# Kernel tuning notes

Measured on AMD Instinct MI355X. Metric: run time of the kernel, lower is better.

## Reference

```python
import jax, jax.numpy as jnp
import numpy as np

N, E, D, L, B = 50000, 800000, 128, 3, 256
BN_EPS = 1e-5


def _bn(h, g, b):
    # BatchNorm1d training-mode math over the node axis (biased variance)
    mu = jnp.mean(h, axis=0)
    var = jnp.mean(jnp.square(h - mu), axis=0)
    return (h - mu) * jax.lax.rsqrt(var + BN_EPS) * g + b


def setup_inputs() -> dict:
    key = jax.random.key(0)
    ks = jax.random.split(key, 6)
    scale = 1.0 / np.sqrt(D).astype(np.float32)
    return {
        "x": jax.random.normal(ks[0], (N, D), dtype=jnp.float32),
        "edge_index": jax.random.randint(ks[1], (2, E), 0, N, dtype=jnp.int32),
        "batch": jnp.sort(jax.random.randint(ks[2], (N,), 0, B, dtype=jnp.int32)),
        "W1": jax.random.normal(ks[3], (L, D, D), dtype=jnp.float32) * scale,
        "b1": jnp.zeros((L, D), jnp.float32),
        "g1": jnp.ones((L, D), jnp.float32),
        "be1": jnp.zeros((L, D), jnp.float32),
        "W2": jax.random.normal(ks[4], (L, D, D), dtype=jnp.float32) * scale,
        "b2": jnp.zeros((L, D), jnp.float32),
        "g2": jnp.ones((L, D), jnp.float32),
        "be2": jnp.zeros((L, D), jnp.float32),
    }


def reference(x, edge_index, batch, W1, b1, g1, be1, W2, b2, g2, be2):
    src, dst = edge_index[0], edge_index[1]
    h = x
    for i in range(L):
        # GINConv (eps=0): h' = nn((1+eps)*h + sum_{j in N(i)} h_j)
        agg = jax.ops.segment_sum(h[src], dst, num_segments=N)  # [N, D]
        h = h + agg
        # nn_layer: Linear -> BN -> ReLU -> Linear
        h = jax.nn.relu(_bn(h @ W1[i] + b1[i], g1[i], be1[i])) @ W2[i] + b2[i]
        # outer BatchNorm + ReLU (dropout is identity in eval)
        h = jax.nn.relu(_bn(h, g2[i], be2[i]))
    # global_add_pool over graphs
    return jax.ops.segment_sum(h, batch, num_segments=B)  # [B, D]
```

## Files before the change

kernel.cpp:

```cpp
#include <hip/hip_runtime.h>

constexpr int kN = 50000;
constexpr int kE = 800000;
constexpr int kD = 128;
constexpr int kB = 256;
constexpr int kL = 3;
constexpr float kEps = 1e-5f;

constexpr int kShift = 7;
constexpr int kNBuk = (kN + 127) >> 7;
constexpr int kEPB = 8192;
constexpr int kNBinBlk = (kE + kEPB - 1) / kEPB;

constexpr int kPxc = kN * kD / 8;
constexpr int kPbnd = kPxc + kN + 1;
constexpr int kPw1 = kPbnd + kL * kD * kD;
constexpr int kPw2 = kPw1 + kL * kD * kD;
constexpr int kPrepThreadBlks = (kPw2 + 255) / 256;

typedef __attribute__((ext_vector_type(8))) short short8;
typedef __attribute__((ext_vector_type(4))) float f32x4;

__device__ __forceinline__ float4 bnrelu4(float4 v, float4 sc, float4 sh) {
  float4 r;
  r.x = fmaxf(fmaf(v.x, sc.x, sh.x), 0.f);
  r.y = fmaxf(fmaf(v.y, sc.y, sh.y), 0.f);
  r.z = fmaxf(fmaf(v.z, sc.z, sh.z), 0.f);
  r.w = fmaxf(fmaf(v.w, sc.w, sh.w), 0.f);
  return r;
}

__device__ __forceinline__ void acc4(float4& a, const float4& v) {
  a.x += v.x; a.y += v.y; a.z += v.z; a.w += v.w;
}
__device__ __forceinline__ void accsq4(float4& a, const float4& v) {
  a.x = fmaf(v.x, v.x, a.x); a.y = fmaf(v.y, v.y, a.y);
  a.z = fmaf(v.z, v.z, a.z); a.w = fmaf(v.w, v.w, a.w);
}

__device__ __forceinline__ unsigned int f2bf(float x) {
  unsigned int u = __float_as_uint(x);
  u = u + 0x7FFFu + ((u >> 16) & 1u);
  return u >> 16;
}
__device__ __forceinline__ float bf2f(unsigned int lo16) {
  return __uint_as_float(lo16 << 16);
}

__device__ __forceinline__ void bnmake(float su, float sq, float ga, float be,
                                       float& sc, float& sh) {
  float mu = su * (1.f / kN);
  float var = fmaf(-mu, mu, sq * (1.f / kN));
  float s = ga * rsqrtf(var + kEps);
  sc = s;
  sh = fmaf(-mu, s, be);
}

__global__ __launch_bounds__(256) void k_prep(
    const float* __restrict__ x, const int* __restrict__ ei,
    const int* __restrict__ bat, const float* __restrict__ W1,
    const float* __restrict__ W2, unsigned short* __restrict__ x16,
    int* __restrict__ bhist, int* __restrict__ gstart,
    unsigned short* __restrict__ Wf1, unsigned short* __restrict__ Wf2) {
  __shared__ int cnt[kNBuk];
  if (blockIdx.x < (unsigned)kNBinBlk) {
    const int tid = threadIdx.x;
    const int e0 = blockIdx.x * kEPB;
    for (int t = tid; t < kNBuk; t += 256) cnt[t] = 0;
    __syncthreads();
#pragma unroll
    for (int i = 0; i < 32; ++i) {
      int e = e0 + i * 256 + tid;
      if (e < kE) atomicAdd(&cnt[ei[kE + e] >> kShift], 1);
    }
    __syncthreads();
    for (int t = tid; t < kNBuk; t += 256) {
      int c = cnt[t];
      if (c) atomicAdd(&bhist[t], c);
    }
    return;
  }
  int idx = (blockIdx.x - kNBinBlk) * 256 + threadIdx.x;
  if (idx < kPxc) {
    const float* ap = x + (size_t)idx * 8;
    float4 v0 = *reinterpret_cast<const float4*>(ap);
    float4 v1 = *reinterpret_cast<const float4*>(ap + 4);
    short8 u;
    u[0] = (short)f2bf(v0.x); u[1] = (short)f2bf(v0.y);
    u[2] = (short)f2bf(v0.z); u[3] = (short)f2bf(v0.w);
    u[4] = (short)f2bf(v1.x); u[5] = (short)f2bf(v1.y);
    u[6] = (short)f2bf(v1.z); u[7] = (short)f2bf(v1.w);
    *reinterpret_cast<short8*>(x16 + (size_t)idx * 8) = u;
  } else if (idx < kPbnd) {
    int n = idx - kPxc;
    int b = (n < kN) ? bat[n] : kB;
    int bp = (n > 0) ? bat[n - 1] : -1;
    for (int g = bp + 1; g <= b; ++g) gstart[g] = n;
  } else if (idx < kPw2) {
    const float* W = (idx < kPw1) ? W1 : W2;
    unsigned short* Wf = (idx < kPw1) ? Wf1 : Wf2;
    int id2 = idx - ((idx < kPw1) ? kPbnd : kPw1);
    int m = id2 & (kD * kD - 1);
    int w = id2 >> 14;
    int k = m >> 7, col = m & 127;
    int kb = k >> 5, cb = col >> 4;
    int lane = (col & 15) + 16 * ((k & 31) >> 3);
    int j = k & 7;
    Wf[(size_t)w * kD * kD + ((size_t)(kb * 8 + cb) * 64 + lane) * 8 + j] =
        (unsigned short)f2bf(W[id2]);
  }
}

__global__ __launch_bounds__(512) void k_scanB(const int* __restrict__ bhist,
                                               int* __restrict__ bstart,
                                               int* __restrict__ bcur) {
  __shared__ int wsum[8];
  const int tid = threadIdx.x;
  const int lane = tid & 63, wid = tid >> 6;
  int v = (tid < kNBuk) ? bhist[tid] : 0;
  int inc = v;
#pragma unroll
  for (int off = 1; off < 64; off <<= 1) {
    int t = __shfl_up(inc, off);
    if (lane >= off) inc += t;
  }
  if (lane == 63) wsum[wid] = inc;
  __syncthreads();
  int wpre = 0;
#pragma unroll
  for (int k = 0; k < 8; ++k) {
    int t = wsum[k];
    if (k < wid) wpre += t;
  }
  int excl = wpre + inc - v;
  if (tid <= kNBuk) {
    bstart[tid] = excl;
    if (tid < kNBuk) bcur[tid] = excl;
  }
}

__global__ __launch_bounds__(256) void k_binpairs(
    const int* __restrict__ ei, int* __restrict__ bcur,
    unsigned int* __restrict__ pairs) {
  __shared__ int cnt[kNBuk];
  __shared__ int base[kNBuk];
  const int tid = threadIdx.x;
  const int e0 = blockIdx.x * kEPB;
  for (int t = tid; t < kNBuk; t += 256) cnt[t] = 0;
  __syncthreads();
  unsigned int dr[32];
#pragma unroll
  for (int i = 0; i < 32; ++i) {
    int e = e0 + i * 256 + tid;
    unsigned int v = 0xFFFFFFFFu;
    if (e < kE) {
      int d = ei[kE + e];
      int r = atomicAdd(&cnt[d >> kShift], 1);
      v = ((unsigned int)d << 16) | (unsigned int)r;
    }
    dr[i] = v;
  }
  __syncthreads();
  for (int t = tid; t < kNBuk; t += 256) {
    int c = cnt[t];
    base[t] = (c > 0) ? atomicAdd(&bcur[t], c) : 0;
  }
  __syncthreads();
#pragma unroll
  for (int i = 0; i < 32; ++i) {
    unsigned int v = dr[i];
    if (v == 0xFFFFFFFFu) continue;
    int e = e0 + i * 256 + tid;
    unsigned int s = (unsigned int)ei[e];
    int b = (int)(v >> 16) >> kShift;
    int pos = base[b] + (int)(v & 0xFFFFu);
    pairs[pos] = (v & 0xFFFF0000u) | s;
  }
}

__global__ __launch_bounds__(256) void k_csrfill(
    const unsigned int* __restrict__ pairs, const int* __restrict__ bstart,
    int* __restrict__ rowptr, int* __restrict__ srcs) {
  __shared__ int cnt[128];
  __shared__ int cur[128];
  __shared__ int w0tot;
  const int b = blockIdx.x;
  const int tid = threadIdx.x;
  const int n0 = b << kShift;
  const int pb = bstart[b];
  const int pe = bstart[b + 1];
  if (tid < 128) cnt[tid] = 0;
  __syncthreads();
  for (int p = pb + tid; p < pe; p += 256)
    atomicAdd(&cnt[(int)(pairs[p] >> 16) - n0], 1);
  __syncthreads();
  int v = 0, inc = 0;
  if (tid < 128) {
    v = cnt[tid];
    inc = v;
#pragma unroll
    for (int off = 1; off < 64; off <<= 1) {
      int t = __shfl_up(inc, off);
      if ((tid & 63) >= off) inc += t;
    }
    if (tid == 63) w0tot = inc;
  }
  __syncthreads();
  if (tid < 128) {
    int excl = inc - v + ((tid >= 64) ? w0tot : 0);
    int n = n0 + tid;
    if (n <= kN) rowptr[n] = pb + excl;
    cur[tid] = pb + excl;
  }
  __syncthreads();
  for (int p = pb + tid; p < pe; p += 256) {
    unsigned int u = pairs[p];
    int local = (int)(u >> 16) - n0;
    int pos = atomicAdd(&cur[local], 1);
    srcs[pos] = (int)(u & 0xFFFFu);
  }
}

template <bool BN>
__global__ __launch_bounds__(256) void k_gather(
    const unsigned int* __restrict__ h16, const int* __restrict__ rowptr,
    const int* __restrict__ srcs, const float* __restrict__ stats,
    const float* __restrict__ gam, const float* __restrict__ bet,
    unsigned int* __restrict__ agg16) {
  const int node = blockIdx.x * 4 + (threadIdx.x >> 6);
  const int lane = threadIdx.x & 63;
  float scx, scy, shx, shy;
  if (BN) {
    int c = lane * 2;
    bnmake(stats[c], stats[kD + c], gam[c], bet[c], scx, shx);
    bnmake(stats[c + 1], stats[kD + c + 1], gam[c + 1], bet[c + 1], scy, shy);
  }
  unsigned int u = h16[(size_t)node * 64 + lane];
  float ax = bf2f(u & 0xFFFFu), ay = __uint_as_float(u & 0xFFFF0000u);
  if (BN) {
    ax = fmaxf(fmaf(ax, scx, shx), 0.f);
    ay = fmaxf(fmaf(ay, scy, shy), 0.f);
  }
  const int beg = __builtin_amdgcn_readfirstlane(rowptr[node]);
  const int end = __builtin_amdgcn_readfirstlane(rowptr[node + 1]);
  int j = beg;
  for (; j + 4 <= end; j += 4) {
    int s0 = srcs[j + 0];
    int s1 = srcs[j + 1];
    int s2 = srcs[j + 2];
    int s3 = srcs[j + 3];
    unsigned int v0 = h16[(size_t)s0 * 64 + lane];
    unsigned int v1 = h16[(size_t)s1 * 64 + lane];
    unsigned int v2 = h16[(size_t)s2 * 64 + lane];
    unsigned int v3 = h16[(size_t)s3 * 64 + lane];
    float x0 = bf2f(v0 & 0xFFFFu), y0 = __uint_as_float(v0 & 0xFFFF0000u);
    float x1 = bf2f(v1 & 0xFFFFu), y1 = __uint_as_float(v1 & 0xFFFF0000u);
    float x2 = bf2f(v2 & 0xFFFFu), y2 = __uint_as_float(v2 & 0xFFFF0000u);
    float x3 = bf2f(v3 & 0xFFFFu), y3 = __uint_as_float(v3 & 0xFFFF0000u);
    if (BN) {
      x0 = fmaxf(fmaf(x0, scx, shx), 0.f); y0 = fmaxf(fmaf(y0, scy, shy), 0.f);
      x1 = fmaxf(fmaf(x1, scx, shx), 0.f); y1 = fmaxf(fmaf(y1, scy, shy), 0.f);
      x2 = fmaxf(fmaf(x2, scx, shx), 0.f); y2 = fmaxf(fmaf(y2, scy, shy), 0.f);
      x3 = fmaxf(fmaf(x3, scx, shx), 0.f); y3 = fmaxf(fmaf(y3, scy, shy), 0.f);
    }
    ax += (x0 + x1) + (x2 + x3);
    ay += (y0 + y1) + (y2 + y3);
  }
  for (; j < end; ++j) {
    int s = srcs[j];
    unsigned int v = h16[(size_t)s * 64 + lane];
    float vx = bf2f(v & 0xFFFFu), vy = __uint_as_float(v & 0xFFFF0000u);
    if (BN) {
      vx = fmaxf(fmaf(vx, scx, shx), 0.f);
      vy = fmaxf(fmaf(vy, scy, shy), 0.f);
    }
    ax += vx;
    ay += vy;
  }
  agg16[(size_t)node * 64 + lane] = f2bf(ax) | (f2bf(ay) << 16);
}

__global__ __launch_bounds__(256) void k_gemm(
    const unsigned short* __restrict__ A16, const unsigned short* __restrict__ Wf,
    const float* __restrict__ bias, const float* __restrict__ statsA,
    const float* __restrict__ gamA, const float* __restrict__ betA,
    unsigned short* __restrict__ Y16,
    float* __restrict__ s_sum, float* __restrict__ s_ss) {
  union SMem {
    unsigned short af[32 * 64 * 8];
    float epi[64 * 132];
  };
  __shared__ SMem sm;

  const int tid = threadIdx.x;
  const int w = tid >> 6;
  const int lane = tid & 63;
  const int row0 = blockIdx.x * 128;

  short8 bfr[4][2];
#pragma unroll
  for (int kb = 0; kb < 4; ++kb)
#pragma unroll
    for (int c = 0; c < 2; ++c)
      bfr[kb][c] = *reinterpret_cast<const short8*>(
          Wf + ((size_t)(kb * 8 + (2 * w + c)) * 64 + lane) * 8);

  {
    const int rlow = tid >> 4;
    const int k0 = (tid & 15) * 8;
    const int kb = k0 >> 5;
    const int lif = rlow + 16 * ((k0 & 31) >> 3);
    float4 sc0, sc1, sh0, sh1;
    if (statsA != nullptr) {
      float4 su0 = *reinterpret_cast<const float4*>(statsA + k0);
      float4 su1 = *reinterpret_cast<const float4*>(statsA + k0 + 4);
      float4 sq0 = *reinterpret_cast<const float4*>(statsA + kD + k0);
      float4 sq1 = *reinterpret_cast<const float4*>(statsA + kD + k0 + 4);
      float4 ga0 = *reinterpret_cast<const float4*>(gamA + k0);
      float4 ga1 = *reinterpret_cast<const float4*>(gamA + k0 + 4);
      float4 be0 = *reinterpret_cast<const float4*>(betA + k0);
      float4 be1 = *reinterpret_cast<const float4*>(betA + k0 + 4);
      bnmake(su0.x, sq0.x, ga0.x, be0.x, sc0.x, sh0.x);
      bnmake(su0.y, sq0.y, ga0.y, be0.y, sc0.y, sh0.y);
      bnmake(su0.z, sq0.z, ga0.z, be0.z, sc0.z, sh0.z);
      bnmake(su0.w, sq0.w, ga0.w, be0.w, sc0.w, sh0.w);
      bnmake(su1.x, sq1.x, ga1.x, be1.x, sc1.x, sh1.x);
      bnmake(su1.y, sq1.y, ga1.y, be1.y, sc1.y, sh1.y);
      bnmake(su1.z, sq1.z, ga1.z, be1.z, sc1.z, sh1.z);
      bnmake(su1.w, sq1.w, ga1.w, be1.w, sc1.w, sh1.w);
    }
#pragma unroll
    for (int i = 0; i < 8; ++i) {
      int grow = row0 + rlow + 16 * i;
      short8 u = (short8)0;
      if (grow < kN) {
        u = *reinterpret_cast<const short8*>(A16 + (size_t)grow * kD + k0);
        if (statsA != nullptr) {
          float4 v0, v1;
          v0.x = bf2f((unsigned short)u[0]); v0.y = bf2f((unsigned short)u[1]);
          v0.z = bf2f((unsigned short)u[2]); v0.w = bf2f((unsigned short)u[3]);
          v1.x = bf2f((unsigned short)u[4]); v1.y = bf2f((unsigned short)u[5]);
          v1.z = bf2f((unsigned short)u[6]); v1.w = bf2f((unsigned short)u[7]);
          v0 = bnrelu4(v0, sc0, sh0);
          v1 = bnrelu4(v1, sc1, sh1);
          u[0] = (short)f2bf(v0.x); u[1] = (short)f2bf(v0.y);
          u[2] = (short)f2bf(v0.z); u[3] = (short)f2bf(v0.w);
          u[4] = (short)f2bf(v1.x); u[5] = (short)f2bf(v1.y);
          u[6] = (short)f2bf(v1.z); u[7] = (short)f2bf(v1.w);
        }
      }
      int frag = i * 4 + kb;
      *reinterpret_cast<short8*>(&sm.af[((size_t)frag * 64 + lif) * 8]) = u;
    }
  }
  __syncthreads();

  f32x4 acc[8][2];
#pragma unroll
  for (int rb = 0; rb < 8; ++rb) {
    acc[rb][0] = (f32x4){0.f, 0.f, 0.f, 0.f};
    acc[rb][1] = (f32x4){0.f, 0.f, 0.f, 0.f};
  }
#pragma unroll
  for (int kb = 0; kb < 4; ++kb) {
    short8 afr[8];
#pragma unroll
    for (int rb = 0; rb < 8; ++rb)
      afr[rb] = *reinterpret_cast<const short8*>(
          &sm.af[((size_t)(rb * 4 + kb) * 64 + lane) * 8]);
#pragma unroll
    for (int rb = 0; rb < 8; ++rb) {
      acc[rb][0] = __builtin_amdgcn_mfma_f32_16x16x32_bf16(afr[rb], bfr[kb][0],
                                                           acc[rb][0], 0, 0, 0);
      acc[rb][1] = __builtin_amdgcn_mfma_f32_16x16x32_bf16(afr[rb], bfr[kb][1],
                                                           acc[rb][1], 0, 0, 0);
    }
  }

  const int col4 = tid & 31;
  const int rowg = tid >> 5;
  float4 b4 = reinterpret_cast<const float4*>(bias)[col4];
  float4 ss = make_float4(0.f, 0.f, 0.f, 0.f);
  float4 qq = make_float4(0.f, 0.f, 0.f, 0.f);

#pragma unroll
  for (int p = 0; p < 2; ++p) {
    __syncthreads();
#pragma unroll
    for (int rb4 = 0; rb4 < 4; ++rb4) {
      int rb = p * 4 + rb4;
#pragma unroll
      for (int c = 0; c < 2; ++c) {
#pragma unroll
        for (int j = 0; j < 4; ++j) {
          sm.epi[(size_t)(rb4 * 16 + (lane >> 4) * 4 + j) * 132 +
                 w * 32 + c * 16 + (lane & 15)] = acc[rb][c][j];
        }
      }
    }
    __syncthreads();
#pragma unroll
    for (int i = 0; i < 8; ++i) {
      int lrow = rowg * 8 + i;
      int grow = row0 + p * 64 + lrow;
      float4 v = *reinterpret_cast<float4*>(&sm.epi[(size_t)lrow * 132 + col4 * 4]);
      acc4(v, b4);
      if (grow < kN) {
        uint2 pk;
        pk.x = f2bf(v.x) | (f2bf(v.y) << 16);
        pk.y = f2bf(v.z) | (f2bf(v.w) << 16);
        *reinterpret_cast<uint2*>(Y16 + (size_t)grow * kD + col4 * 4) = pk;
        acc4(ss, v);
        accsq4(qq, v);
      }
    }
  }

  __syncthreads();
  *reinterpret_cast<float4*>(&sm.epi[(size_t)rowg * 128 + col4 * 4]) = ss;
  *reinterpret_cast<float4*>(&sm.epi[1024 + (size_t)rowg * 128 + col4 * 4]) = qq;
  __syncthreads();
  if (tid < kD) {
    float s = 0.f;
#pragma unroll
    for (int j = 0; j < 8; ++j) s += sm.epi[j * 128 + tid];
    atomicAdd(&s_sum[tid], s);
  } else {
    int c = tid - kD;
    float s = 0.f;
#pragma unroll
    for (int j = 0; j < 8; ++j) s += sm.epi[1024 + j * 128 + c];
    atomicAdd(&s_ss[c], s);
  }
}

__global__ __launch_bounds__(256) void k_pool(
    const unsigned short* __restrict__ h16, const int* __restrict__ gstart,
    const float* __restrict__ stats, const float* __restrict__ gam,
    const float* __restrict__ bet, float* __restrict__ out) {
  const int g = blockIdx.x;
  const int q = threadIdx.x & 31;
  const int r = threadIdx.x >> 5;
  const int s = gstart[g], e = gstart[g + 1];
  float4 sc, sh;
  {
    int c = q * 4;
    bnmake(stats[c + 0], stats[kD + c + 0], gam[c + 0], bet[c + 0], sc.x, sh.x);
    bnmake(stats[c + 1], stats[kD + c + 1], gam[c + 1], bet[c + 1], sc.y, sh.y);
    bnmake(stats[c + 2], stats[kD + c + 2], gam[c + 2], bet[c + 2], sc.z, sh.z);
    bnmake(stats[c + 3], stats[kD + c + 3], gam[c + 3], bet[c + 3], sc.w, sh.w);
  }
  float4 acc = make_float4(0.f, 0.f, 0.f, 0.f);
  for (int n = s + r; n < e; n += 8) {
    uint2 u = *reinterpret_cast<const uint2*>(h16 + (size_t)n * kD + q * 4);
    float4 v;
    v.x = bf2f(u.x & 0xFFFFu);
    v.y = __uint_as_float(u.x & 0xFFFF0000u);
    v.z = bf2f(u.y & 0xFFFFu);
    v.w = __uint_as_float(u.y & 0xFFFF0000u);
    acc4(acc, bnrelu4(v, sc, sh));
  }
  __shared__ float4 red[8][32];
  red[r][q] = acc;
  __syncthreads();
  if (r == 0) {
    float4 t = acc;
#pragma unroll
    for (int j = 1; j < 8; ++j) acc4(t, red[j][q]);
    reinterpret_cast<float4*>(out)[(size_t)g * 32 + q] = t;
  }
}

extern "C" void kernel_launch(void* const* d_in, const int* in_sizes, int n_in,
                              void* d_out, int out_size, void* d_ws, size_t ws_size,
                              hipStream_t stream) {
  const float* x   = (const float*)d_in[0];
  const int*   ei  = (const int*)d_in[1];
  const int*   bat = (const int*)d_in[2];
  const float* W1  = (const float*)d_in[3];
  const float* b1  = (const float*)d_in[4];
  const float* g1  = (const float*)d_in[5];
  const float* be1 = (const float*)d_in[6];
  const float* W2  = (const float*)d_in[7];
  const float* b2  = (const float*)d_in[8];
  const float* g2  = (const float*)d_in[9];
  const float* be2 = (const float*)d_in[10];
  float* out = (float*)d_out;

  char* p = (char*)d_ws;
  float* wsf = (float*)p;                       p += 16384;
  unsigned short* x16 = (unsigned short*)p;     p += (size_t)kN * kD * 2;
  unsigned short* bufA = (unsigned short*)p;    p += (size_t)kN * kD * 2;
  unsigned short* bufB = (unsigned short*)p;    p += (size_t)kN * kD * 2;
  unsigned short* Wf1 = (unsigned short*)p;     p += (size_t)kL * kD * kD * 2;
  unsigned short* Wf2 = (unsigned short*)p;     p += (size_t)kL * kD * kD * 2;
  int* rowptr = (int*)p;                        p += (kN + 2) * 4;
  int* bhist = (int*)p;                         p += (kNBuk + 1) * 4;
  int* bstart = (int*)p;                        p += (kNBuk + 1) * 4;
  int* bcur = (int*)p;                          p += (kNBuk + 1) * 4;
  int* gstart = (int*)p;                        p += (kB + 2) * 4;
  unsigned int* pairs = (unsigned int*)p;       p += (size_t)kE * 4;
  int* srcs = (int*)p;                          p += (size_t)kE * 4;

  (void)hipMemsetAsync(wsf, 0, 6 * 512 * sizeof(float), stream);
  (void)hipMemsetAsync(bhist, 0, kNBuk * sizeof(int), stream);

  k_prep<<<kNBinBlk + kPrepThreadBlks, 256, 0, stream>>>(x, ei, bat, W1, W2, x16,
                                                         bhist, gstart, Wf1, Wf2);
  k_scanB<<<1, 512, 0, stream>>>(bhist, bstart, bcur);
  k_binpairs<<<kNBinBlk, 256, 0, stream>>>(ei, bcur, pairs);
  k_csrfill<<<kNBuk, 256, 0, stream>>>(pairs, bstart, rowptr, srcs);

  const unsigned short* curH = x16;
  const float* curStats = nullptr;
  const float* curGam = nullptr;
  const float* curBet = nullptr;
  const int ngemm = (kN + 127) / 128;

  unsigned short* aggBuf = bufA;
  unsigned short* yBuf = bufB;

  for (int l = 0; l < kL; ++l) {
    if (curStats == nullptr)
      k_gather<false><<<kN / 4, 256, 0, stream>>>(
          (const unsigned int*)curH, rowptr, srcs, nullptr, nullptr, nullptr,
          (unsigned int*)aggBuf);
    else
      k_gather<true><<<kN / 4, 256, 0, stream>>>(
          (const unsigned int*)curH, rowptr, srcs, curStats, curGam, curBet,
          (unsigned int*)aggBuf);

    float* st1 = wsf + (size_t)(l * 2 + 0) * 512;
    k_gemm<<<ngemm, 256, 0, stream>>>(aggBuf, Wf1 + (size_t)l * kD * kD,
                                      b1 + l * kD, nullptr, nullptr, nullptr,
                                      yBuf, st1, st1 + kD);

    float* st2 = wsf + (size_t)(l * 2 + 1) * 512;
    k_gemm<<<ngemm, 256, 0, stream>>>(yBuf, Wf2 + (size_t)l * kD * kD,
                                      b2 + l * kD, st1, g1 + l * kD, be1 + l * kD,
                                      aggBuf, st2, st2 + kD);

    curH = aggBuf;
    curStats = st2;
    curGam = g2 + l * kD;
    curBet = be2 + l * kD;
    unsigned short* tmp = aggBuf;
    aggBuf = yBuf;
    yBuf = tmp;
  }

  k_pool<<<kB, 256, 0, stream>>>(curH, gstart, curStats, curGam, curBet, out);
}
```

Measured before the change: 293.6 us.

## Fuse neighbor gather into first GEMM and drop memsets and global histogram atomics

The separate gather kernel is replaced by k_gemmg, which aggregates each node's neighbors straight into LDS as bf16 MFMA A-fragments and then runs the first linear layer. This removes one kernel launch per layer and the round trip of the aggregated tensor through global memory. The edge-bucket histogram now writes per-block counts that the scan kernel sums, replacing global atomics, and the stats buffer is zeroed inside k_prep instead of by two memset calls. The gather now uses 16 lanes per row with uint4 loads, so memory-level parallelism changes and the MFMA stage waits on irregular gather latency within each block.

```diff
diff --git a/kernel.cpp b/kernel.cpp
--- a/kernel.cpp
+++ b/kernel.cpp
@@ -16,7 +16,8 @@
 constexpr int kPbnd = kPxc + kN + 1;
 constexpr int kPw1 = kPbnd + kL * kD * kD;
 constexpr int kPw2 = kPw1 + kL * kD * kD;
-constexpr int kPrepThreadBlks = (kPw2 + 255) / 256;
+constexpr int kPzero = kPw2 + 768;
+constexpr int kPrepThreadBlks = (kPzero + 255) / 256;
 
 typedef __attribute__((ext_vector_type(8))) short short8;
 typedef __attribute__((ext_vector_type(4))) float f32x4;
@@ -46,6 +47,9 @@
 __device__ __forceinline__ float bf2f(unsigned int lo16) {
   return __uint_as_float(lo16 << 16);
 }
+__device__ __forceinline__ float bfhi(unsigned int u) {
+  return __uint_as_float(u & 0xFFFF0000u);
+}
 
 __device__ __forceinline__ void bnmake(float su, float sq, float ga, float be,
                                        float& sc, float& sh) {
@@ -56,12 +60,34 @@
   sh = fmaf(-mu, s, be);
 }
 
+template <bool BN>
+__device__ __forceinline__ void rowadd(float* a, uint4 v, const float* sc,
+                                       const float* sh) {
+  float t0 = bf2f(v.x & 0xFFFFu), t1 = bfhi(v.x);
+  float t2 = bf2f(v.y & 0xFFFFu), t3 = bfhi(v.y);
+  float t4 = bf2f(v.z & 0xFFFFu), t5 = bfhi(v.z);
+  float t6 = bf2f(v.w & 0xFFFFu), t7 = bfhi(v.w);
+  if (BN) {
+    t0 = fmaxf(fmaf(t0, sc[0], sh[0]), 0.f);
+    t1 = fmaxf(fmaf(t1, sc[1], sh[1]), 0.f);
+    t2 = fmaxf(fmaf(t2, sc[2], sh[2]), 0.f);
+    t3 = fmaxf(fmaf(t3, sc[3], sh[3]), 0.f);
+    t4 = fmaxf(fmaf(t4, sc[4], sh[4]), 0.f);
+    t5 = fmaxf(fmaf(t5, sc[5], sh[5]), 0.f);
+    t6 = fmaxf(fmaf(t6, sc[6], sh[6]), 0.f);
+    t7 = fmaxf(fmaf(t7, sc[7], sh[7]), 0.f);
+  }
+  a[0] += t0; a[1] += t1; a[2] += t2; a[3] += t3;
+  a[4] += t4; a[5] += t5; a[6] += t6; a[7] += t7;
+}
+
 __global__ __launch_bounds__(256) void k_prep(
     const float* __restrict__ x, const int* __restrict__ ei,
     const int* __restrict__ bat, const float* __restrict__ W1,
     const float* __restrict__ W2, unsigned short* __restrict__ x16,
-    int* __restrict__ bhist, int* __restrict__ gstart,
-    unsigned short* __restrict__ Wf1, unsigned short* __restrict__ Wf2) {
+    int* __restrict__ bcnt, int* __restrict__ gstart,
+    unsigned short* __restrict__ Wf1, unsigned short* __restrict__ Wf2,
+    float* __restrict__ wsf) {
   __shared__ int cnt[kNBuk];
   if (blockIdx.x < (unsigned)kNBinBlk) {
     const int tid = threadIdx.x;
@@ -74,10 +100,8 @@
       if (e < kE) atomicAdd(&cnt[ei[kE + e] >> kShift], 1);
     }
     __syncthreads();
-    for (int t = tid; t < kNBuk; t += 256) {
-      int c = cnt[t];
-      if (c) atomicAdd(&bhist[t], c);
-    }
+    for (int t = tid; t < kNBuk; t += 256)
+      bcnt[blockIdx.x * kNBuk + t] = cnt[t];
     return;
   }
   int idx = (blockIdx.x - kNBinBlk) * 256 + threadIdx.x;
@@ -108,16 +132,22 @@
     int j = k & 7;
     Wf[(size_t)w * kD * kD + ((size_t)(kb * 8 + cb) * 64 + lane) * 8 + j] =
         (unsigned short)f2bf(W[id2]);
-  }
-}
-
-__global__ __launch_bounds__(512) void k_scanB(const int* __restrict__ bhist,
+  } else if (idx < kPzero) {
+    int z = idx - kPw2;
+    reinterpret_cast<float4*>(wsf)[z] = make_float4(0.f, 0.f, 0.f, 0.f);
+  }
+}
+
+__global__ __launch_bounds__(512) void k_scanB(const int* __restrict__ bcnt,
                                                int* __restrict__ bstart,
                                                int* __restrict__ bcur) {
   __shared__ int wsum[8];
   const int tid = threadIdx.x;
   const int lane = tid & 63, wid = tid >> 6;
-  int v = (tid < kNBuk) ? bhist[tid] : 0;
+  int v = 0;
+  if (tid < kNBuk) {
+    for (int blk = 0; blk < kNBinBlk; ++blk) v += bcnt[blk * kNBuk + tid];
+  }
   int inc = v;
 #pragma unroll
   for (int off = 1; off < 64; off <<= 1) {
@@ -222,62 +252,154 @@
 }
 
 template <bool BN>
-__global__ __launch_bounds__(256) void k_gather(
+__global__ __launch_bounds__(256) void k_gemmg(
     const unsigned int* __restrict__ h16, const int* __restrict__ rowptr,
-    const int* __restrict__ srcs, const float* __restrict__ stats,
+    const int* __restrict__ srcs, const unsigned short* __restrict__ Wf,
+    const float* __restrict__ bias, const float* __restrict__ stats,
     const float* __restrict__ gam, const float* __restrict__ bet,
-    unsigned int* __restrict__ agg16) {
-  const int node = blockIdx.x * 4 + (threadIdx.x >> 6);
-  const int lane = threadIdx.x & 63;
-  float scx, scy, shx, shy;
+    unsigned short* __restrict__ Y16,
+    float* __restrict__ s_sum, float* __restrict__ s_ss) {
+  union SMem {
+    unsigned short af[32 * 64 * 8];
+    float epi[64 * 132];
+  };
+  __shared__ SMem sm;
+
+  const int tid = threadIdx.x;
+  const int w = tid >> 6;
+  const int lane = tid & 63;
+  const int row0 = blockIdx.x * 128;
+
+  const int rlow = tid >> 4;
+  const int c4 = tid & 15;
+  const int kb = c4 >> 2;
+  const int lif = rlow + 16 * (c4 & 3);
+
+  float sc[8], sh[8];
   if (BN) {
-    int c = lane * 2;
-    bnmake(stats[c], stats[kD + c], gam[c], bet[c], scx, shx);
-    bnmake(stats[c + 1], stats[kD + c + 1], gam[c + 1], bet[c + 1], scy, shy);
-  }
-  unsigned int u = h16[(size_t)node * 64 + lane];
-  float ax = bf2f(u & 0xFFFFu), ay = __uint_as_float(u & 0xFFFF0000u);
-  if (BN) {
-    ax = fmaxf(fmaf(ax, scx, shx), 0.f);
-    ay = fmaxf(fmaf(ay, scy, shy), 0.f);
-  }
-  const int beg = __builtin_amdgcn_readfirstlane(rowptr[node]);
-  const int end = __builtin_amdgcn_readfirstlane(rowptr[node + 1]);
-  int j = beg;
-  for (; j + 4 <= end; j += 4) {
-    int s0 = srcs[j + 0];
-    int s1 = srcs[j + 1];
-    int s2 = srcs[j + 2];
-    int s3 = srcs[j + 3];
-    unsigned int v0 = h16[(size_t)s0 * 64 + lane];
-    unsigned int v1 = h16[(size_t)s1 * 64 + lane];
-    unsigned int v2 = h16[(size_t)s2 * 64 + lane];
-    unsigned int v3 = h16[(size_t)s3 * 64 + lane];
-    float x0 = bf2f(v0 & 0xFFFFu), y0 = __uint_as_float(v0 & 0xFFFF0000u);
-    float x1 = bf2f(v1 & 0xFFFFu), y1 = __uint_as_float(v1 & 0xFFFF0000u);
-    float x2 = bf2f(v2 & 0xFFFFu), y2 = __uint_as_float(v2 & 0xFFFF0000u);
-    float x3 = bf2f(v3 & 0xFFFFu), y3 = __uint_as_float(v3 & 0xFFFF0000u);
-    if (BN) {
-      x0 = fmaxf(fmaf(x0, scx, shx), 0.f); y0 = fmaxf(fmaf(y0, scy, shy), 0.f);
-      x1 = fmaxf(fmaf(x1, scx, shx), 0.f); y1 = fmaxf(fmaf(y1, scy, shy), 0.f);
-      x2 = fmaxf(fmaf(x2, scx, shx), 0.f); y2 = fmaxf(fmaf(y2, scy, shy), 0.f);
-      x3 = fmaxf(fmaf(x3, scx, shx), 0.f); y3 = fmaxf(fmaf(y3, scy, shy), 0.f);
-    }
-    ax += (x0 + x1) + (x2 + x3);
-    ay += (y0 + y1) + (y2 + y3);
-  }
-  for (; j < end; ++j) {
-    int s = srcs[j];
-    unsigned int v = h16[(size_t)s * 64 + lane];
-    float vx = bf2f(v & 0xFFFFu), vy = __uint_as_float(v & 0xFFFF0000u);
-    if (BN) {
-      vx = fmaxf(fmaf(vx, scx, shx), 0.f);
-      vy = fmaxf(fmaf(vy, scy, shy), 0.f);
-    }
-    ax += vx;
-    ay += vy;
-  }
-  agg16[(size_t)node * 64 + lane] = f2bf(ax) | (f2bf(ay) << 16);
+    int k0 = c4 * 8;
+#pragma unroll
+    for (int q = 0; q < 8; ++q)
+      bnmake(stats[k0 + q], stats[kD + k0 + q], gam[k0 + q], bet[k0 + q],
+             sc[q], sh[q]);
+  }
+
+#pragma unroll
+  for (int i = 0; i < 8; ++i) {
+    int row = row0 + rlow + 16 * i;
+    float a[8] = {0.f, 0.f, 0.f, 0.f, 0.f, 0.f, 0.f, 0.f};
+    if (row < kN) {
+      uint4 vs = *reinterpret_cast<const uint4*>(h16 + (size_t)row * 64 + c4 * 4);
+      rowadd<BN>(a, vs, sc, sh);
+      int beg = rowptr[row];
+      int end = rowptr[row + 1];
+      int j = beg;
+      for (; j + 2 <= end; j += 2) {
+        int s0 = srcs[j];
+        int s1 = srcs[j + 1];
+        uint4 v0 = *reinterpret_cast<const uint4*>(h16 + (size_t)s0 * 64 + c4 * 4);
+        uint4 v1 = *reinterpret_cast<const uint4*>(h16 + (size_t)s1 * 64 + c4 * 4);
+        rowadd<BN>(a, v0, sc, sh);
+        rowadd<BN>(a, v1, sc, sh);
+      }
+      if (j < end) {
+        int s0 = srcs[j];
+        uint4 v0 = *reinterpret_cast<const uint4*>(h16 + (size_t)s0 * 64 + c4 * 4);
+        rowadd<BN>(a, v0, sc, sh);
+      }
+    }
+    short8 u;
+#pragma unroll
+    for (int q = 0; q < 8; ++q) u[q] = (short)f2bf(a[q]);
+    *reinterpret_cast<short8*>(&sm.af[((size_t)(i * 4 + kb) * 64 + lif) * 8]) = u;
+  }
+
+  short8 bfr[4][2];
+#pragma unroll
+  for (int kk = 0; kk < 4; ++kk)
+#pragma unroll
+    for (int c = 0; c < 2; ++c)
+      bfr[kk][c] = *reinterpret_cast<const short8*>(
+          Wf + ((size_t)(kk * 8 + (2 * w + c)) * 64 + lane) * 8);
+  __syncthreads();
+
+  f32x4 acc[8][2];
+#pragma unroll
+  for (int rb = 0; rb < 8; ++rb) {
+    acc[rb][0] = (f32x4){0.f, 0.f, 0.f, 0.f};
+    acc[rb][1] = (f32x4){0.f, 0.f, 0.f, 0.f};
+  }
+#pragma unroll
+  for (int kk = 0; kk < 4; ++kk) {
+    short8 afr[8];
+#pragma unroll
+    for (int rb = 0; rb < 8; ++rb)
+      afr[rb] = *reinterpret_cast<const short8*>(
+          &sm.af[((size_t)(rb * 4 + kk) * 64 + lane) * 8]);
+#pragma unroll
+    for (int rb = 0; rb < 8; ++rb) {
+      acc[rb][0] = __builtin_amdgcn_mfma_f32_16x16x32_bf16(afr[rb], bfr[kk][0],
+                                                           acc[rb][0], 0, 0, 0);
+      acc[rb][1] = __builtin_amdgcn_mfma_f32_16x16x32_bf16(afr[rb], bfr[kk][1],
+                                                           acc[rb][1], 0, 0, 0);
+    }
+  }
+
+  const int col4 = tid & 31;
+  const int rowg = tid >> 5;
+  float4 b4 = reinterpret_cast<const float4*>(bias)[col4];
+  float4 ss = make_float4(0.f, 0.f, 0.f, 0.f);
+  float4 qq = make_float4(0.f, 0.f, 0.f, 0.f);
+
+#pragma unroll
+  for (int p = 0; p < 2; ++p) {
+    __syncthreads();
+#pragma unroll
+    for (int rb4 = 0; rb4 < 4; ++rb4) {
+      int rb = p * 4 + rb4;
+#pragma unroll
+      for (int c = 0; c < 2; ++c) {
+#pragma unroll
+        for (int j = 0; j < 4; ++j) {
+          sm.epi[(size_t)(rb4 * 16 + (lane >> 4) * 4 + j) * 132 +
+                 w * 32 + c * 16 + (lane & 15)] = acc[rb][c][j];
+        }
+      }
+    }
+    __syncthreads();
+#pragma unroll
+    for (int i = 0; i < 8; ++i) {
+      int lrow = rowg * 8 + i;
+      int grow = row0 + p * 64 + lrow;
+      float4 v = *reinterpret_cast<float4*>(&sm.epi[(size_t)lrow * 132 + col4 * 4]);
+      acc4(v, b4);
+      if (grow < kN) {
+        uint2 pk;
+        pk.x = f2bf(v.x) | (f2bf(v.y) << 16);
+        pk.y = f2bf(v.z) | (f2bf(v.w) << 16);
+        *reinterpret_cast<uint2*>(Y16 + (size_t)grow * kD + col4 * 4) = pk;
+        acc4(ss, v);
+        accsq4(qq, v);
+      }
+    }
+  }
+
+  __syncthreads();
+  *reinterpret_cast<float4*>(&sm.epi[(size_t)rowg * 128 + col4 * 4]) = ss;
+  *reinterpret_cast<float4*>(&sm.epi[1024 + (size_t)rowg * 128 + col4 * 4]) = qq;
+  __syncthreads();
+  if (tid < kD) {
+    float s = 0.f;
+#pragma unroll
+    for (int j = 0; j < 8; ++j) s += sm.epi[j * 128 + tid];
+    atomicAdd(&s_sum[tid], s);
+  } else {
+    int c = tid - kD;
+    float s = 0.f;
+#pragma unroll
+    for (int j = 0; j < 8; ++j) s += sm.epi[1024 + j * 128 + c];
+    atomicAdd(&s_ss[c], s);
+  }
 }
 
 __global__ __launch_bounds__(256) void k_gemm(
@@ -311,7 +433,7 @@
     const int kb = k0 >> 5;
     const int lif = rlow + 16 * ((k0 & 31) >> 3);
     float4 sc0, sc1, sh0, sh1;
-    if (statsA != nullptr) {
+    {
       float4 su0 = *reinterpret_cast<const float4*>(statsA + k0);
       float4 su1 = *reinterpret_cast<const float4*>(statsA + k0 + 4);
       float4 sq0 = *reinterpret_cast<const float4*>(statsA + kD + k0);
@@ -335,19 +457,17 @@
       short8 u = (short8)0;
       if (grow < kN) {
         u = *reinterpret_cast<const short8*>(A16 + (size_t)grow * kD + k0);
-        if (statsA != nullptr) {
-          float4 v0, v1;
-          v0.x = bf2f((unsigned short)u[0]); v0.y = bf2f((unsigned short)u[1]);
-          v0.z = bf2f((unsigned short)u[2]); v0.w = bf2f((unsigned short)u[3]);
-          v1.x = bf2f((unsigned short)u[4]); v1.y = bf2f((unsigned short)u[5]);
-          v1.z = bf2f((unsigned short)u[6]); v1.w = bf2f((unsigned short)u[7]);
-          v0 = bnrelu4(v0, sc0, sh0);
-          v1 = bnrelu4(v1, sc1, sh1);
-          u[0] = (short)f2bf(v0.x); u[1] = (short)f2bf(v0.y);
-          u[2] = (short)f2bf(v0.z); u[3] = (short)f2bf(v0.w);
-          u[4] = (short)f2bf(v1.x); u[5] = (short)f2bf(v1.y);
-          u[6] = (short)f2bf(v1.z); u[7] = (short)f2bf(v1.w);
-        }
+        float4 v0, v1;
+        v0.x = bf2f((unsigned short)u[0]); v0.y = bf2f((unsigned short)u[1]);
+        v0.z = bf2f((unsigned short)u[2]); v0.w = bf2f((unsigned short)u[3]);
+        v1.x = bf2f((unsigned short)u[4]); v1.y = bf2f((unsigned short)u[5]);
+        v1.z = bf2f((unsigned short)u[6]); v1.w = bf2f((unsigned short)u[7]);
+        v0 = bnrelu4(v0, sc0, sh0);
+        v1 = bnrelu4(v1, sc1, sh1);
+        u[0] = (short)f2bf(v0.x); u[1] = (short)f2bf(v0.y);
+        u[2] = (short)f2bf(v0.z); u[3] = (short)f2bf(v0.w);
+        u[4] = (short)f2bf(v1.x); u[5] = (short)f2bf(v1.y);
+        u[6] = (short)f2bf(v1.z); u[7] = (short)f2bf(v1.w);
       }
       int frag = i * 4 + kb;
       *reinterpret_cast<short8*>(&sm.af[((size_t)frag * 64 + lif) * 8]) = u;
@@ -495,19 +615,16 @@
   unsigned short* Wf1 = (unsigned short*)p;     p += (size_t)kL * kD * kD * 2;
   unsigned short* Wf2 = (unsigned short*)p;     p += (size_t)kL * kD * kD * 2;
   int* rowptr = (int*)p;                        p += (kN + 2) * 4;
-  int* bhist = (int*)p;                         p += (kNBuk + 1) * 4;
   int* bstart = (int*)p;                        p += (kNBuk + 1) * 4;
   int* bcur = (int*)p;                          p += (kNBuk + 1) * 4;
   int* gstart = (int*)p;                        p += (kB + 2) * 4;
+  int* bcnt = (int*)p;                          p += (size_t)kNBinBlk * kNBuk * 4;
   unsigned int* pairs = (unsigned int*)p;       p += (size_t)kE * 4;
   int* srcs = (int*)p;                          p += (size_t)kE * 4;
 
-  (void)hipMemsetAsync(wsf, 0, 6 * 512 * sizeof(float), stream);
-  (void)hipMemsetAsync(bhist, 0, kNBuk * sizeof(int), stream);
-
-  k_prep<<<kNBinBlk + kPrepThreadBlks, 256, 0, stream>>>(x, ei, bat, W1, W2, x16,
-                                                         bhist, gstart, Wf1, Wf2);
-  k_scanB<<<1, 512, 0, stream>>>(bhist, bstart, bcur);
+  k_prep<<<kNBinBlk + kPrepThreadBlks, 256, 0, stream>>>(
+      x, ei, bat, W1, W2, x16, bcnt, gstart, Wf1, Wf2, wsf);
+  k_scanB<<<1, 512, 0, stream>>>(bcnt, bstart, bcur);
   k_binpairs<<<kNBinBlk, 256, 0, stream>>>(ei, bcur, pairs);
   k_csrfill<<<kNBuk, 256, 0, stream>>>(pairs, bstart, rowptr, srcs);
 
@@ -517,36 +634,29 @@
   const float* curBet = nullptr;
   const int ngemm = (kN + 127) / 128;
 
-  unsigned short* aggBuf = bufA;
-  unsigned short* yBuf = bufB;
-
   for (int l = 0; l < kL; ++l) {
+    unsigned short* y1 = bufA;
+    unsigned short* y2 = (l & 1) ? x16 : bufB;
+
+    float* st1 = wsf + (size_t)(l * 2 + 0) * 512;
     if (curStats == nullptr)
-      k_gather<false><<<kN / 4, 256, 0, stream>>>(
-          (const unsigned int*)curH, rowptr, srcs, nullptr, nullptr, nullptr,
-          (unsigned int*)aggBuf);
+      k_gemmg<false><<<ngemm, 256, 0, stream>>>(
+          (const unsigned int*)curH, rowptr, srcs, Wf1 + (size_t)l * kD * kD,
+          b1 + l * kD, nullptr, nullptr, nullptr, y1, st1, st1 + kD);
     else
-      k_gather<true><<<kN / 4, 256, 0, stream>>>(
-          (const unsigned int*)curH, rowptr, srcs, curStats, curGam, curBet,
-          (unsigned int*)aggBuf);
-
-    float* st1 = wsf + (size_t)(l * 2 + 0) * 512;
-    k_gemm<<<ngemm, 256, 0, stream>>>(aggBuf, Wf1 + (size_t)l * kD * kD,
-                                      b1 + l * kD, nullptr, nullptr, nullptr,
-                                      yBuf, st1, st1 + kD);
+      k_gemmg<true><<<ngemm, 256, 0, stream>>>(
+          (const unsigned int*)curH, rowptr, srcs, Wf1 + (size_t)l * kD * kD,
+          b1 + l * kD, curStats, curGam, curBet, y1, st1, st1 + kD);
 
     float* st2 = wsf + (size_t)(l * 2 + 1) * 512;
-    k_gemm<<<ngemm, 256, 0, stream>>>(yBuf, Wf2 + (size_t)l * kD * kD,
+    k_gemm<<<ngemm, 256, 0, stream>>>(y1, Wf2 + (size_t)l * kD * kD,
                                       b2 + l * kD, st1, g1 + l * kD, be1 + l * kD,
-                                      aggBuf, st2, st2 + kD);
-
-    curH = aggBuf;
+                                      y2, st2, st2 + kD);
+
+    curH = y2;
     curStats = st2;
     curGam = g2 + l * kD;
     curBet = be2 + l * kD;
-    unsigned short* tmp = aggBuf;
-    aggBuf = yBuf;
-    yBuf = tmp;
   }
 
   k_pool<<<kB, 256, 0, stream>>>(curH, gstart, curStats, curGam, curBet, out);
```

Measured after the change: 370.1 us. 1.26x slower.

## Drop memsets, use per-block bucket counts, unroll gather by 8, template GEMM

Applied to the files above, without the earlier changes.

Removes the two hipMemsetAsync calls: k_prep now zeroes the stats workspace itself, and it writes per-block bucket histograms that k_scanB sums, so no global atomics are needed. The gather loop now issues 8 masked loads per iteration with clamped indices, which adds memory-level parallelism. The GEMM BN path is made a compile-time template parameter. Buffers are reused in fixed roles, with x16 serving as the running h. The cost is a serial 98-block sum in the scan and some wasted loads on nodes with low degree.

```diff
diff --git a/kernel.cpp b/kernel.cpp
--- a/kernel.cpp
+++ b/kernel.cpp
@@ -16,7 +16,8 @@
 constexpr int kPbnd = kPxc + kN + 1;
 constexpr int kPw1 = kPbnd + kL * kD * kD;
 constexpr int kPw2 = kPw1 + kL * kD * kD;
-constexpr int kPrepThreadBlks = (kPw2 + 255) / 256;
+constexpr int kPzero = kPw2 + 768;
+constexpr int kPrepThreadBlks = (kPzero + 255) / 256;
 
 typedef __attribute__((ext_vector_type(8))) short short8;
 typedef __attribute__((ext_vector_type(4))) float f32x4;
@@ -46,6 +47,9 @@
 __device__ __forceinline__ float bf2f(unsigned int lo16) {
   return __uint_as_float(lo16 << 16);
 }
+__device__ __forceinline__ float bfhi(unsigned int u) {
+  return __uint_as_float(u & 0xFFFF0000u);
+}
 
 __device__ __forceinline__ void bnmake(float su, float sq, float ga, float be,
                                        float& sc, float& sh) {
@@ -60,8 +64,9 @@
     const float* __restrict__ x, const int* __restrict__ ei,
     const int* __restrict__ bat, const float* __restrict__ W1,
     const float* __restrict__ W2, unsigned short* __restrict__ x16,
-    int* __restrict__ bhist, int* __restrict__ gstart,
-    unsigned short* __restrict__ Wf1, unsigned short* __restrict__ Wf2) {
+    int* __restrict__ bcnt, int* __restrict__ gstart,
+    unsigned short* __restrict__ Wf1, unsigned short* __restrict__ Wf2,
+    float* __restrict__ wsf) {
   __shared__ int cnt[kNBuk];
   if (blockIdx.x < (unsigned)kNBinBlk) {
     const int tid = threadIdx.x;
@@ -74,10 +79,8 @@
       if (e < kE) atomicAdd(&cnt[ei[kE + e] >> kShift], 1);
     }
     __syncthreads();
-    for (int t = tid; t < kNBuk; t += 256) {
-      int c = cnt[t];
-      if (c) atomicAdd(&bhist[t], c);
-    }
+    for (int t = tid; t < kNBuk; t += 256)
+      bcnt[blockIdx.x * kNBuk + t] = cnt[t];
     return;
   }
   int idx = (blockIdx.x - kNBinBlk) * 256 + threadIdx.x;
@@ -108,16 +111,22 @@
     int j = k & 7;
     Wf[(size_t)w * kD * kD + ((size_t)(kb * 8 + cb) * 64 + lane) * 8 + j] =
         (unsigned short)f2bf(W[id2]);
-  }
-}
-
-__global__ __launch_bounds__(512) void k_scanB(const int* __restrict__ bhist,
+  } else if (idx < kPzero) {
+    int z = idx - kPw2;
+    reinterpret_cast<float4*>(wsf)[z] = make_float4(0.f, 0.f, 0.f, 0.f);
+  }
+}
+
+__global__ __launch_bounds__(512) void k_scanB(const int* __restrict__ bcnt,
                                                int* __restrict__ bstart,
                                                int* __restrict__ bcur) {
   __shared__ int wsum[8];
   const int tid = threadIdx.x;
   const int lane = tid & 63, wid = tid >> 6;
-  int v = (tid < kNBuk) ? bhist[tid] : 0;
+  int v = 0;
+  if (tid < kNBuk) {
+    for (int blk = 0; blk < kNBinBlk; ++blk) v += bcnt[blk * kNBuk + tid];
+  }
   int inc = v;
 #pragma unroll
   for (int off = 1; off < 64; off <<= 1) {
@@ -236,50 +245,37 @@
     bnmake(stats[c + 1], stats[kD + c + 1], gam[c + 1], bet[c + 1], scy, shy);
   }
   unsigned int u = h16[(size_t)node * 64 + lane];
-  float ax = bf2f(u & 0xFFFFu), ay = __uint_as_float(u & 0xFFFF0000u);
+  float ax = bf2f(u & 0xFFFFu), ay = bfhi(u);
   if (BN) {
     ax = fmaxf(fmaf(ax, scx, shx), 0.f);
     ay = fmaxf(fmaf(ay, scy, shy), 0.f);
   }
   const int beg = __builtin_amdgcn_readfirstlane(rowptr[node]);
   const int end = __builtin_amdgcn_readfirstlane(rowptr[node + 1]);
-  int j = beg;
-  for (; j + 4 <= end; j += 4) {
-    int s0 = srcs[j + 0];
-    int s1 = srcs[j + 1];
-    int s2 = srcs[j + 2];
-    int s3 = srcs[j + 3];
-    unsigned int v0 = h16[(size_t)s0 * 64 + lane];
-    unsigned int v1 = h16[(size_t)s1 * 64 + lane];
-    unsigned int v2 = h16[(size_t)s2 * 64 + lane];
-    unsigned int v3 = h16[(size_t)s3 * 64 + lane];
-    float x0 = bf2f(v0 & 0xFFFFu), y0 = __uint_as_float(v0 & 0xFFFF0000u);
-    float x1 = bf2f(v1 & 0xFFFFu), y1 = __uint_as_float(v1 & 0xFFFF0000u);
-    float x2 = bf2f(v2 & 0xFFFFu), y2 = __uint_as_float(v2 & 0xFFFF0000u);
-    float x3 = bf2f(v3 & 0xFFFFu), y3 = __uint_as_float(v3 & 0xFFFF0000u);
-    if (BN) {
-      x0 = fmaxf(fmaf(x0, scx, shx), 0.f); y0 = fmaxf(fmaf(y0, scy, shy), 0.f);
-      x1 = fmaxf(fmaf(x1, scx, shx), 0.f); y1 = fmaxf(fmaf(y1, scy, shy), 0.f);
-      x2 = fmaxf(fmaf(x2, scx, shx), 0.f); y2 = fmaxf(fmaf(y2, scy, shy), 0.f);
-      x3 = fmaxf(fmaf(x3, scx, shx), 0.f); y3 = fmaxf(fmaf(y3, scy, shy), 0.f);
-    }
-    ax += (x0 + x1) + (x2 + x3);
-    ay += (y0 + y1) + (y2 + y3);
-  }
-  for (; j < end; ++j) {
-    int s = srcs[j];
-    unsigned int v = h16[(size_t)s * 64 + lane];
-    float vx = bf2f(v & 0xFFFFu), vy = __uint_as_float(v & 0xFFFF0000u);
-    if (BN) {
-      vx = fmaxf(fmaf(vx, scx, shx), 0.f);
-      vy = fmaxf(fmaf(vy, scy, shy), 0.f);
-    }
-    ax += vx;
-    ay += vy;
+  const int last = end - 1;
+  for (int j0 = beg; j0 < end; j0 += 8) {
+    unsigned int v[8];
+#pragma unroll
+    for (int q = 0; q < 8; ++q) {
+      int s = srcs[min(j0 + q, last)];
+      v[q] = h16[(size_t)s * 64 + lane];
+    }
+#pragma unroll
+    for (int q = 0; q < 8; ++q) {
+      float vx = bf2f(v[q] & 0xFFFFu), vy = bfhi(v[q]);
+      if (BN) {
+        vx = fmaxf(fmaf(vx, scx, shx), 0.f);
+        vy = fmaxf(fmaf(vy, scy, shy), 0.f);
+      }
+      bool ok = (j0 + q) < end;
+      ax += ok ? vx : 0.f;
+      ay += ok ? vy : 0.f;
+    }
   }
   agg16[(size_t)node * 64 + lane] = f2bf(ax) | (f2bf(ay) << 16);
 }
 
+template <bool BN>
 __global__ __launch_bounds__(256) void k_gemm(
     const unsigned short* __restrict__ A16, const unsigned short* __restrict__ Wf,
     const float* __restrict__ bias, const float* __restrict__ statsA,
@@ -311,7 +307,7 @@
     const int kb = k0 >> 5;
     const int lif = rlow + 16 * ((k0 & 31) >> 3);
     float4 sc0, sc1, sh0, sh1;
-    if (statsA != nullptr) {
+    if (BN) {
       float4 su0 = *reinterpret_cast<const float4*>(statsA + k0);
       float4 su1 = *reinterpret_cast<const float4*>(statsA + k0 + 4);
       float4 sq0 = *reinterpret_cast<const float4*>(statsA + kD + k0);
@@ -335,7 +331,7 @@
       short8 u = (short8)0;
       if (grow < kN) {
         u = *reinterpret_cast<const short8*>(A16 + (size_t)grow * kD + k0);
-        if (statsA != nullptr) {
+        if (BN) {
           float4 v0, v1;
           v0.x = bf2f((unsigned short)u[0]); v0.y = bf2f((unsigned short)u[1]);
           v0.z = bf2f((unsigned short)u[2]); v0.w = bf2f((unsigned short)u[3]);
@@ -455,9 +451,9 @@
     uint2 u = *reinterpret_cast<const uint2*>(h16 + (size_t)n * kD + q * 4);
     float4 v;
     v.x = bf2f(u.x & 0xFFFFu);
-    v.y = __uint_as_float(u.x & 0xFFFF0000u);
+    v.y = bfhi(u.x);
     v.z = bf2f(u.y & 0xFFFFu);
-    v.w = __uint_as_float(u.y & 0xFFFF0000u);
+    v.w = bfhi(u.y);
     acc4(acc, bnrelu4(v, sc, sh));
   }
   __shared__ float4 red[8][32];
@@ -495,59 +491,49 @@
   unsigned short* Wf1 = (unsigned short*)p;     p += (size_t)kL * kD * kD * 2;
   unsigned short* Wf2 = (unsigned short*)p;     p += (size_t)kL * kD * kD * 2;
   int* rowptr = (int*)p;                        p += (kN + 2) * 4;
-  int* bhist = (int*)p;                         p += (kNBuk + 1) * 4;
   int* bstart = (int*)p;                        p += (kNBuk + 1) * 4;
   int* bcur = (int*)p;                          p += (kNBuk + 1) * 4;
   int* gstart = (int*)p;                        p += (kB + 2) * 4;
+  int* bcnt = (int*)p;                          p += (size_t)kNBinBlk * kNBuk * 4;
   unsigned int* pairs = (unsigned int*)p;       p += (size_t)kE * 4;
   int* srcs = (int*)p;                          p += (size_t)kE * 4;
 
-  (void)hipMemsetAsync(wsf, 0, 6 * 512 * sizeof(float), stream);
-  (void)hipMemsetAsync(bhist, 0, kNBuk * sizeof(int), stream);
-
-  k_prep<<<kNBinBlk + kPrepThreadBlks, 256, 0, stream>>>(x, ei, bat, W1, W2, x16,
-                                                         bhist, gstart, Wf1, Wf2);
-  k_scanB<<<1, 512, 0, stream>>>(bhist, bstart, bcur);
+  k_prep<<<kNBinBlk + kPrepThreadBlks, 256, 0, stream>>>(
+      x, ei, bat, W1, W2, x16, bcnt, gstart, Wf1, Wf2, wsf);
+  k_scanB<<<1, 512, 0, stream>>>(bcnt, bstart, bcur);
   k_binpairs<<<kNBinBlk, 256, 0, stream>>>(ei, bcur, pairs);
   k_csrfill<<<kNBuk, 256, 0, stream>>>(pairs, bstart, rowptr, srcs);
 
-  const unsigned short* curH = x16;
   const float* curStats = nullptr;
   const float* curGam = nullptr;
   const float* curBet = nullptr;
   const int ngemm = (kN + 127) / 128;
 
-  unsigned short* aggBuf = bufA;
-  unsigned short* yBuf = bufB;
-
   for (int l = 0; l < kL; ++l) {
+    float* st1 = wsf + (size_t)(l * 2 + 0) * 512;
+    float* st2 = wsf + (size_t)(l * 2 + 1) * 512;
+
     if (curStats == nullptr)
       k_gather<false><<<kN / 4, 256, 0, stream>>>(
-          (const unsigned int*)curH, rowptr, srcs, nullptr, nullptr, nullptr,
-          (unsigned int*)aggBuf);
+          (const unsigned int*)x16, rowptr, srcs, nullptr, nullptr, nullptr,
+          (unsigned int*)bufA);
     else
       k_gather<true><<<kN / 4, 256, 0, stream>>>(
-          (const unsigned int*)curH, rowptr, srcs, curStats, curGam, curBet,
-          (unsigned int*)aggBuf);
-
-    float* st1 = wsf + (size_t)(l * 2 + 0) * 512;
-    k_gemm<<<ngemm, 256, 0, stream>>>(aggBuf, Wf1 + (size_t)l * kD * kD,
-                                      b1 + l * kD, nullptr, nullptr, nullptr,
-                                      yBuf, st1, st1 + kD);
-
-    float* st2 = wsf + (size_t)(l * 2 + 1) * 512;
-    k_gemm<<<ngemm, 256, 0, stream>>>(yBuf, Wf2 + (size_t)l * kD * kD,
-                                      b2 + l * kD, st1, g1 + l * kD, be1 + l * kD,
-                                      aggBuf, st2, st2 + kD);
-
-    curH = aggBuf;
+          (const unsigned int*)x16, rowptr, srcs, curStats, curGam, curBet,
+          (unsigned int*)bufA);
+
+    k_gemm<false><<<ngemm, 256, 0, stream>>>(bufA, Wf1 + (size_t)l * kD * kD,
+                                             b1 + l * kD, nullptr, nullptr,
+                                             nullptr, bufB, st1, st1 + kD);
+
+    k_gemm<true><<<ngemm, 256, 0, stream>>>(bufB, Wf2 + (size_t)l * kD * kD,
+                                            b2 + l * kD, st1, g1 + l * kD,
+                                            be1 + l * kD, x16, st2, st2 + kD);
+
     curStats = st2;
     curGam = g2 + l * kD;
     curBet = be2 + l * kD;
-    unsigned short* tmp = aggBuf;
-    aggBuf = yBuf;
-    yBuf = tmp;
-  }
-
-  k_pool<<<kB, 256, 0, stream>>>(curH, gstart, curStats, curGam, curBet, out);
-}
+  }
+
+  k_pool<<<kB, 256, 0, stream>>>(x16, gstart, curStats, curGam, curBet, out);
+}
```

Result: faster. 276.2 us, median of 2 (-5.9%).
